# Kernel tuning notes

Measured on AMD Instinct MI355X. Metric: run time of the kernel, lower is better.

The kernel has to match this reference:

```python
import jax, jax.numpy as jnp
import numpy as np

B, T_TEXT, T_AUDIO, D = 16, 512, 4096, 256
TEMPERATURE = 10.0


def setup_inputs() -> dict:
    key = jax.random.key(0)
    k1, k2 = jax.random.split(key)
    hidden_state = jax.random.normal(k1, (B, D, T_TEXT), dtype=jnp.float32)
    # monotone token centers in [0, T_AUDIO)
    centers = jnp.sort(
        jax.random.uniform(k2, (B, T_TEXT), dtype=jnp.float32, minval=0.0, maxval=float(T_AUDIO)),
        axis=-1,
    )
    # audio frame timestamps 0..A-1, shared across batch
    audio_timestamps = jnp.broadcast_to(
        jnp.arange(T_AUDIO, dtype=jnp.float32), (B, T_AUDIO)
    )
    return {
        "hidden_state": hidden_state,
        "centers": centers,
        "audio_timestamps": audio_timestamps,
    }


def reference(hidden_state, centers, audio_timestamps):
    # interpolation_weights: squared-distance score, temperature-scaled softmax over tokens
    # centers: [B, T], audio_timestamps: [B, A] -> diffs: [B, A, T]
    diffs = centers[:, None, :] - audio_timestamps[:, :, None]
    logits = (-(TEMPERATURE ** -2)) * jnp.square(diffs)  # [B, A, T]
    weights = jax.nn.softmax(logits, axis=-1)            # softmax over token dim
    # audio_aligned_representation: matmul + sum reduction, fused into one einsum
    # hidden_state: [B, D, T]; contract T with weights, then sum over audio axis A
    out = jnp.einsum("bdt,bat->bd", hidden_state, weights)
    return out
```

## Files before the change

kernel.cpp:

```cpp
#include <hip/hip_runtime.h>

#define B_ 16
#define T_ 512
#define A_ 4096
#define D_ 256
#define NEG_SCALE2 (-0.01f * 1.4426950408889634f)
#define CHUNK 256
#define RADIUS 96.0f

__global__ __launch_bounds__(256) void k_weights(const float* __restrict__ centers,
                                                 const float* __restrict__ ats,
                                                 float* __restrict__ wsum) {
    __shared__ float  sc[T_];
    __shared__ float2 ai[CHUNK];

    const int tid = threadIdx.x;
    const int b  = blockIdx.y;
    const int a0 = blockIdx.x * CHUNK;

    const float c0 = centers[b * T_ + tid];
    const float c1 = centers[b * T_ + tid + 256];
    sc[tid]       = c0;
    sc[tid + 256] = c1;
    const float myts = ats[b * A_ + a0 + tid];
    ai[tid] = make_float2(myts, 0.f);
    __syncthreads();

    const float lov = ai[0].x - RADIUS;
    const float hiv = ai[CHUNK - 1].x + RADIUS;
    const int tlo = __syncthreads_count(c0 < lov) + __syncthreads_count(c1 < lov);
    const int thi = T_ - __syncthreads_count(c0 > hiv) - __syncthreads_count(c1 > hiv);

    float s0 = 0.f, s1 = 0.f;
    int t = tlo;
    #pragma unroll 4
    for (; t + 1 < thi; t += 2) {
        float d0 = sc[t] - myts;
        float d1 = sc[t + 1] - myts;
        s0 += __builtin_exp2f(NEG_SCALE2 * d0 * d0);
        s1 += __builtin_exp2f(NEG_SCALE2 * d1 * d1);
    }
    if (t < thi) {
        float d = sc[t] - myts;
        s0 += __builtin_exp2f(NEG_SCALE2 * d * d);
    }
    ai[tid].y = 1.0f / fmaxf(s0 + s1, 1e-37f);
    __syncthreads();

    for (int base = tlo; base < thi; base += 64) {
        int tt = base + (tid >> 2);
        if (tt < thi) {
            float c = sc[tt];
            float w0 = 0.f, w1 = 0.f;
            #pragma unroll 4
            for (int k = (tid & 3); k < CHUNK; k += 8) {
                float2 p = ai[k];
                float dp = c - p.x;
                w0 += __builtin_exp2f(NEG_SCALE2 * dp * dp) * p.y;
                float2 q = ai[k + 4];
                float dq = c - q.x;
                w1 += __builtin_exp2f(NEG_SCALE2 * dq * dq) * q.y;
            }
            float w = w0 + w1;
            w += __shfl_xor(w, 1, 64);
            w += __shfl_xor(w, 2, 64);
            if ((tid & 3) == 0) atomicAdd(&wsum[b * T_ + tt], w);
        }
    }
}

__global__ __launch_bounds__(256) void k_out(const float* __restrict__ hidden,
                                             const float* __restrict__ wsum,
                                             float* __restrict__ out) {
    const int tid  = threadIdx.x;
    const int lane = tid & 63;
    const int wave = tid >> 6;
    const int o = blockIdx.x * 4 + wave;
    const int b = o >> 8;

    const float4* hp = (const float4*)(hidden + (size_t)o * T_);
    const float4* wp = (const float4*)(wsum + (size_t)b * T_);

    float acc = 0.f;
    #pragma unroll
    for (int i = 0; i < 2; ++i) {
        float4 h = hp[lane + i * 64];
        float4 w = wp[lane + i * 64];
        acc += h.x * w.x + h.y * w.y + h.z * w.z + h.w * w.w;
    }
    #pragma unroll
    for (int off = 32; off; off >>= 1)
        acc += __shfl_down(acc, off, 64);
    if (lane == 0) out[o] = acc;
}

extern "C" void kernel_launch(void* const* d_in, const int* in_sizes, int n_in,
                              void* d_out, int out_size, void* d_ws, size_t ws_size,
                              hipStream_t stream) {
    const float* hidden  = (const float*)d_in[0];
    const float* centers = (const float*)d_in[1];
    const float* ats     = (const float*)d_in[2];
    float* out  = (float*)d_out;
    float* wsum = (float*)d_ws;

    k_weights<<<dim3(A_ / CHUNK, B_), 256, 0, stream>>>(centers, ats, wsum);
    k_out<<<(B_ * D_) / 4, 256, 0, stream>>>(hidden, wsum, out);
}
```

Measured before the change: 68.37 us.

## Fuse weight computation and hidden-state contraction into one kernel

Merges the two kernels into one. Each block keeps its partial per-token weight sums in shared memory instead of atomically adding them into a global workspace. Each thread then dots one hidden-state row over the block's active token window and atomically adds the result into the output. This drops a kernel launch and the global wsum round trip, and only touches hidden entries inside each chunk's token window. The cost is strided, poorly coalesced per-thread row reads, more atomics on the output, and a reliance on the output buffer being zero-initialised.

Result: slower. 70.67 us (+3.4%).

```diff
diff --git a/kernel.cpp b/kernel.cpp
--- a/kernel.cpp
+++ b/kernel.cpp
@@ -8,11 +8,13 @@
 #define CHUNK 256
 #define RADIUS 96.0f
 
-__global__ __launch_bounds__(256) void k_weights(const float* __restrict__ centers,
+__global__ __launch_bounds__(256) void k_aligner(const float* __restrict__ centers,
                                                  const float* __restrict__ ats,
-                                                 float* __restrict__ wsum) {
+                                                 const float* __restrict__ hidden,
+                                                 float* __restrict__ out) {
     __shared__ float  sc[T_];
     __shared__ float2 ai[CHUNK];
+    __shared__ float  wl[T_];
 
     const int tid = threadIdx.x;
     const int b  = blockIdx.y;
@@ -22,6 +24,8 @@
     const float c1 = centers[b * T_ + tid + 256];
     sc[tid]       = c0;
     sc[tid + 256] = c1;
+    wl[tid]       = 0.f;
+    wl[tid + 256] = 0.f;
     const float myts = ats[b * A_ + a0 + tid];
     ai[tid] = make_float2(myts, 0.f);
     __syncthreads();
@@ -64,34 +68,32 @@
             float w = w0 + w1;
             w += __shfl_xor(w, 1, 64);
             w += __shfl_xor(w, 2, 64);
-            if ((tid & 3) == 0) atomicAdd(&wsum[b * T_ + tt], w);
+            if ((tid & 3) == 0) wl[tt] = w;
         }
     }
-}
+    __syncthreads();
 
-__global__ __launch_bounds__(256) void k_out(const float* __restrict__ hidden,
-                                             const float* __restrict__ wsum,
-                                             float* __restrict__ out) {
-    const int tid  = threadIdx.x;
-    const int lane = tid & 63;
-    const int wave = tid >> 6;
-    const int o = blockIdx.x * 4 + wave;
-    const int b = o >> 8;
+    const int t4lo = tlo & ~3;
+    const int t4hi = (thi + 3) & ~3;
+    const float* hrow = hidden + (size_t)(b * D_ + tid) * T_;
+    const float4* wl4 = (const float4*)wl;
 
-    const float4* hp = (const float4*)(hidden + (size_t)o * T_);
-    const float4* wp = (const float4*)(wsum + (size_t)b * T_);
-
-    float acc = 0.f;
-    #pragma unroll
-    for (int i = 0; i < 2; ++i) {
-        float4 h = hp[lane + i * 64];
-        float4 w = wp[lane + i * 64];
-        acc += h.x * w.x + h.y * w.y + h.z * w.z + h.w * w.w;
+    float accA = 0.f, accB = 0.f;
+    int tt = t4lo;
+    for (; tt + 4 < t4hi; tt += 8) {
+        float4 h0 = *(const float4*)(hrow + tt);
+        float4 w0 = wl4[tt >> 2];
+        accA += h0.x * w0.x + h0.y * w0.y + h0.z * w0.z + h0.w * w0.w;
+        float4 h1 = *(const float4*)(hrow + tt + 4);
+        float4 w1 = wl4[(tt >> 2) + 1];
+        accB += h1.x * w1.x + h1.y * w1.y + h1.z * w1.z + h1.w * w1.w;
     }
-    #pragma unroll
-    for (int off = 32; off; off >>= 1)
-        acc += __shfl_down(acc, off, 64);
-    if (lane == 0) out[o] = acc;
+    if (tt < t4hi) {
+        float4 h0 = *(const float4*)(hrow + tt);
+        float4 w0 = wl4[tt >> 2];
+        accA += h0.x * w0.x + h0.y * w0.y + h0.z * w0.z + h0.w * w0.w;
+    }
+    atomicAdd(&out[b * D_ + tid], accA + accB);
 }
 
 extern "C" void kernel_launch(void* const* d_in, const int* in_sizes, int n_in,
@@ -101,8 +103,6 @@
     const float* centers = (const float*)d_in[1];
     const float* ats     = (const float*)d_in[2];
     float* out  = (float*)d_out;
-    float* wsum = (float*)d_ws;
 
-    k_weights<<<dim3(A_ / CHUNK, B_), 256, 0, stream>>>(centers, ats, wsum);
-    k_out<<<(B_ * D_) / 4, 256, 0, stream>>>(hidden, wsum, out);
+    k_aligner<<<dim3(A_ / CHUNK, B_), 256, 0, stream>>>(centers, ats, hidden, out);
 }
```
